# Optimization experiments

Measured on AMD Instinct MI355X. Metric: run time of the kernel, lower is better.

## Reference

```python
import jax, jax.numpy as jnp
import numpy as np

N_NODES = 500_000
N_EDGES = 16_000_000
N_COLORS = 64


def _mix(v, c1, c2):
    """32-bit integer hash (lowbias32-style avalanche mix)."""
    v = v.astype(jnp.uint32)
    v = (v ^ (v >> 16)) * jnp.uint32(c1)
    v = (v ^ (v >> 13)) * jnp.uint32(c2)
    return v ^ (v >> 16)


def setup_inputs() -> dict:
    key = jax.random.key(0)
    k1, k2 = jax.random.split(key)
    x = jax.random.randint(k1, (N_NODES,), 0, N_COLORS, dtype=jnp.int32)
    edge_index = jax.random.randint(k2, (2, N_EDGES), 0, N_NODES, dtype=jnp.int32)
    return {"x": x, "edge_index": edge_index}


def reference(x, edge_index):
    """One Weisfeiler-Lehman color-refinement step.

    Faithful semantics of WLConvOptimized.forward: each node's new label is
    determined by the equivalence class of (own label, multiset of incoming
    neighbor labels). Instead of Python tuple-sort + hash()+dict, we use a
    permutation-invariant multiset hash (sum of two independent 32-bit hashes
    of neighbor labels, combined with the node's own label hash) and then a
    sort-based dense relabeling. Nodes get equal output labels iff their
    (label, neighbor-multiset) signatures collide -- same partition as the
    original (up to astronomically unlikely hash collisions); label numbering
    is canonical (sorted-signature order) rather than dict-insertion order.
    """
    num_nodes = x.shape[0]
    row, col = edge_index[0], edge_index[1]  # message flows row (src) -> col (dst)

    # two independent per-label hashes
    ha = _mix(x, 0x045D9F3B, 0x045D9F3B)
    hb = _mix(x, 0x9E3779B1, 0x85EBCA77)

    # permutation-invariant multiset hash of incoming neighbor labels (gather + scatter-add)
    sum_a = jnp.zeros(num_nodes, jnp.uint32).at[col].add(ha[row])
    sum_b = jnp.zeros(num_nodes, jnp.uint32).at[col].add(hb[row])

    # combine own label with neighbor multiset, re-avalanche
    sig_a = _mix(ha * jnp.uint32(0x27D4EB2F) + sum_a, 0xC2B2AE3D, 0x165667B1)
    sig_b = _mix(hb * jnp.uint32(0x61C88647) + sum_b, 0x045D9F3B, 0x27D4EB2F)

    # dense relabel: sort by (sig_a, sig_b), number distinct signatures 0..K-1
    order = jnp.lexsort((sig_b, sig_a))
    sa, sb = sig_a[order], sig_b[order]
    new_grp = jnp.concatenate([
        jnp.zeros(1, jnp.int32),
        ((sa[1:] != sa[:-1]) | (sb[1:] != sb[:-1])).astype(jnp.int32),
    ])
    labels_sorted = jnp.cumsum(new_grp).astype(jnp.int32)
    out = jnp.zeros(num_nodes, jnp.int32).at[order].set(labels_sorted)
    return out
```

## Files before the change

kernel.cpp:

```cpp
#include <hip/hip_runtime.h>
#include <stdint.h>

#define LOG_B 17
#define NB (1u << LOG_B)
#define FINE_NODES 1024
#define NBKT 512
#define CSH 10
#define EPB 16384

__host__ __device__ constexpr uint32_t cmix(uint32_t v, uint32_t c1, uint32_t c2) {
    v = (v ^ (v >> 16)) * c1;
    v = (v ^ (v >> 13)) * c2;
    return v ^ (v >> 16);
}

__device__ __forceinline__ uint32_t mixh(uint32_t v, uint32_t c1, uint32_t c2) {
    v = (v ^ (v >> 16)) * c1;
    v = (v ^ (v >> 13)) * c2;
    return v ^ (v >> 16);
}

struct Luts { uint32_t ha[64]; uint32_t hb[64]; };
constexpr Luts make_luts() {
    Luts l{};
    for (uint32_t i = 0; i < 64; i++) {
        l.ha[i] = cmix(i, 0x045D9F3Bu, 0x045D9F3Bu);
        l.hb[i] = cmix(i, 0x9E3779B1u, 0x85EBCA77u);
    }
    return l;
}
__constant__ Luts LUT = make_luts();

__global__ __launch_bounds__(256) void k_bin(const int* __restrict__ row, const int* __restrict__ col,
                                             const int* __restrict__ x, uint16_t* __restrict__ bins,
                                             uint32_t* __restrict__ cursor, int E, int cap) {
    __shared__ uint16_t stage[EPB];
    __shared__ uint32_t hist[NBKT];
    __shared__ uint16_t gb16[NBKT];
    __shared__ uint32_t wsum[4];
    int t = threadIdx.x;
    int lane = t & 63, wid = t >> 6;
    int base = blockIdx.x * EPB;
    int nend = min(E - base, EPB);
    for (int b = t; b < NBKT; b += 256) hist[b] = 0;
    __syncthreads();

    const int4* col4 = (const int4*)(col + base);
    const int4* row4 = (const int4*)(row + base);
    int n4 = nend >> 2;

    for (int k = t; k < n4; k += 256) {
        int4 c = col4[k];
        atomicAdd(&hist[(uint32_t)c.x >> CSH], 1u);
        atomicAdd(&hist[(uint32_t)c.y >> CSH], 1u);
        atomicAdd(&hist[(uint32_t)c.z >> CSH], 1u);
        atomicAdd(&hist[(uint32_t)c.w >> CSH], 1u);
    }
    for (int k = (n4 << 2) + t; k < nend; k += 256)
        atomicAdd(&hist[(uint32_t)col[base + k] >> CSH], 1u);
    __syncthreads();

    int b0 = 2 * t;
    uint32_t h0 = hist[b0], h1 = hist[b0 + 1];
    uint32_t s = h0 + h1;
    uint32_t inc = s;
    for (int off = 1; off < 64; off <<= 1) {
        uint32_t nv = __shfl_up(inc, (unsigned)off, 64);
        if (lane >= off) inc += nv;
    }
    if (lane == 63) wsum[wid] = inc;
    __syncthreads();
    uint32_t woff = 0;
    for (int w = 0; w < wid; w++) woff += wsum[w];
    uint32_t e0 = woff + inc - s;
    uint32_t g0 = h0 ? atomicAdd(&cursor[b0], h0) : 0u;
    uint32_t g1 = h1 ? atomicAdd(&cursor[b0 + 1], h1) : 0u;
    gb16[b0] = (uint16_t)g0;
    gb16[b0 + 1] = (uint16_t)g1;
    hist[b0] = e0 << 16;
    hist[b0 + 1] = (e0 + h0) << 16;
    __syncthreads();

    for (int k = t; k < n4; k += 256) {
        int4 c = col4[k];
        int4 r = row4[k];
        {
            uint32_t d = (uint32_t)c.x, b = d >> CSH;
            uint32_t o = atomicAdd(&hist[b], 1u);
            stage[(o >> 16) + (o & 0xFFFFu)] = (uint16_t)(((d & 1023u) << 6) | (uint32_t)x[r.x]);
        }
        {
            uint32_t d = (uint32_t)c.y, b = d >> CSH;
            uint32_t o = atomicAdd(&hist[b], 1u);
            stage[(o >> 16) + (o & 0xFFFFu)] = (uint16_t)(((d & 1023u) << 6) | (uint32_t)x[r.y]);
        }
        {
            uint32_t d = (uint32_t)c.z, b = d >> CSH;
            uint32_t o = atomicAdd(&hist[b], 1u);
            stage[(o >> 16) + (o & 0xFFFFu)] = (uint16_t)(((d & 1023u) << 6) | (uint32_t)x[r.z]);
        }
        {
            uint32_t d = (uint32_t)c.w, b = d >> CSH;
            uint32_t o = atomicAdd(&hist[b], 1u);
            stage[(o >> 16) + (o & 0xFFFFu)] = (uint16_t)(((d & 1023u) << 6) | (uint32_t)x[r.w]);
        }
    }
    for (int k = (n4 << 2) + t; k < nend; k += 256) {
        int i = base + k;
        uint32_t d = (uint32_t)col[i], b = d >> CSH;
        uint32_t o = atomicAdd(&hist[b], 1u);
        stage[(o >> 16) + (o & 0xFFFFu)] = (uint16_t)(((d & 1023u) << 6) | (uint32_t)x[row[i]]);
    }
    __syncthreads();

    int sub = lane >> 4, l16 = lane & 15;
    for (int b = wid * 4 + sub; b < NBKT; b += 16) {
        uint32_t hv = hist[b];
        uint32_t cnt = hv & 0xFFFFu;
        if (!cnt) continue;
        uint32_t s0 = hv >> 16;
        uint16_t* dst = bins + (size_t)b * (uint32_t)cap + gb16[b];
        for (uint32_t off = l16; off < cnt; off += 16)
            dst[off] = stage[s0 + off];
    }
}

__global__ __launch_bounds__(256) void k_accsig(const uint16_t* __restrict__ bins,
                                                const uint32_t* __restrict__ cursor,
                                                const int* __restrict__ x,
                                                unsigned long long* __restrict__ sigs,
                                                uint32_t* __restrict__ bcnt, int N, int cap) {
    __shared__ uint32_t cnt[FINE_NODES * 16];
    int t = threadIdx.x;
    int b = blockIdx.x;
    for (int i = t; i < FINE_NODES * 16; i += 256) cnt[i] = 0;
    __syncthreads();
    uint32_t m = cursor[b];
    const uint16_t* mybins = bins + (size_t)b * (uint32_t)cap;
    const uint2* p16v = (const uint2*)mybins;
    uint32_t m4 = m >> 2;
    for (uint32_t k = t; k < m4; k += 256) {
        uint2 rv = p16v[k];
        {
            uint32_t rec = rv.x & 0xFFFFu, n = rec >> 6, c = rec & 63u;
            atomicAdd(&cnt[n * 16 + (c >> 2)], 1u << (8u * (c & 3u)));
        }
        {
            uint32_t rec = rv.x >> 16, n = rec >> 6, c = rec & 63u;
            atomicAdd(&cnt[n * 16 + (c >> 2)], 1u << (8u * (c & 3u)));
        }
        {
            uint32_t rec = rv.y & 0xFFFFu, n = rec >> 6, c = rec & 63u;
            atomicAdd(&cnt[n * 16 + (c >> 2)], 1u << (8u * (c & 3u)));
        }
        {
            uint32_t rec = rv.y >> 16, n = rec >> 6, c = rec & 63u;
            atomicAdd(&cnt[n * 16 + (c >> 2)], 1u << (8u * (c & 3u)));
        }
    }
    for (uint32_t k = (m4 << 2) + t; k < m; k += 256) {
        uint32_t rec = mybins[k], n = rec >> 6, c = rec & 63u;
        atomicAdd(&cnt[n * 16 + (c >> 2)], 1u << (8u * (c & 3u)));
    }
    __syncthreads();

    for (int n = t; n < FINE_NODES; n += 256) {
        int g = b * FINE_NODES + n;
        if (g >= N) break;
        uint32_t sum_a = 0, sum_b = 0;
#pragma unroll
        for (int w = 0; w < 16; w++) {
            uint32_t wp = (uint32_t)(w + n) & 15u;
            uint32_t v = cnt[n * 16 + wp];
            uint32_t c0 = v & 255u, c1 = (v >> 8) & 255u, c2 = (v >> 16) & 255u, c3 = v >> 24;
            sum_a += c0 * LUT.ha[4 * wp] + c1 * LUT.ha[4 * wp + 1]
                   + c2 * LUT.ha[4 * wp + 2] + c3 * LUT.ha[4 * wp + 3];
            sum_b += c0 * LUT.hb[4 * wp] + c1 * LUT.hb[4 * wp + 1]
                   + c2 * LUT.hb[4 * wp + 2] + c3 * LUT.hb[4 * wp + 3];
        }
        uint32_t xv = (uint32_t)x[g];
        uint32_t ha = LUT.ha[xv];
        uint32_t hb = LUT.hb[xv];
        uint32_t sa = mixh(ha * 0x27D4EB2Fu + sum_a, 0xC2B2AE3Du, 0x165667B1u);
        uint32_t sb = mixh(hb * 0x61C88647u + sum_b, 0x045D9F3Bu, 0x27D4EB2Fu);
        unsigned long long key = ((unsigned long long)sa << 32) | (unsigned long long)sb;
        sigs[g] = key;
        atomicAdd(&bcnt[(uint32_t)(key >> (64 - LOG_B))], 1u);
    }
}

__global__ void k_scan1(const uint32_t* __restrict__ in, uint32_t* __restrict__ out,
                        uint32_t* __restrict__ part) {
    __shared__ uint32_t s[1024];
    int t = threadIdx.x;
    int idx = blockIdx.x * 1024 + t;
    uint32_t v = in[idx];
    s[t] = v;
    __syncthreads();
    for (int off = 1; off < 1024; off <<= 1) {
        uint32_t add = (t >= off) ? s[t - off] : 0u;
        __syncthreads();
        s[t] += add;
        __syncthreads();
    }
    out[idx] = s[t] - v;
    if (t == 1023) part[blockIdx.x] = s[t];
}

__global__ void k_scan2(uint32_t* __restrict__ part) {
    __shared__ uint32_t s[256];
    int t = threadIdx.x;
    uint32_t v = part[t];
    s[t] = v;
    __syncthreads();
    for (int off = 1; off < 256; off <<= 1) {
        uint32_t add = (t >= off) ? s[t - off] : 0u;
        __syncthreads();
        s[t] += add;
        __syncthreads();
    }
    part[t] = s[t] - v;
}

__global__ void k_scan3(uint32_t* __restrict__ out, const uint32_t* __restrict__ part) {
    int idx = blockIdx.x * 1024 + threadIdx.x;
    out[idx] += part[blockIdx.x];
}

__global__ void k_scatter(const unsigned long long* __restrict__ sigs,
                          const uint32_t* __restrict__ boff, uint32_t* __restrict__ bcur,
                          unsigned long long* __restrict__ skey, uint32_t* __restrict__ snode,
                          int N) {
    int i = blockIdx.x * blockDim.x + threadIdx.x;
    if (i >= N) return;
    unsigned long long key = sigs[i];
    uint32_t b = (uint32_t)(key >> (64 - LOG_B));
    uint32_t pos = boff[b] + atomicAdd(&bcur[b], 1u);
    skey[pos] = key;
    snode[pos] = (uint32_t)i;
}

__global__ void k_bsort(unsigned long long* __restrict__ skey, uint32_t* __restrict__ snode,
                        const uint32_t* __restrict__ boff, uint32_t* __restrict__ ldx,
                        uint32_t* __restrict__ dcnt, int N) {
    int b = blockIdx.x * blockDim.x + threadIdx.x;
    if (b >= (int)NB) return;
    uint32_t s0 = boff[b];
    uint32_t s1 = (b == (int)NB - 1) ? (uint32_t)N : boff[b + 1];
    for (uint32_t i = s0 + 1; i < s1; i++) {
        unsigned long long k = skey[i];
        uint32_t nd = snode[i];
        uint32_t j = i;
        while (j > s0 && skey[j - 1] > k) {
            skey[j] = skey[j - 1];
            snode[j] = snode[j - 1];
            j--;
        }
        skey[j] = k;
        snode[j] = nd;
    }
    uint32_t d = 0;
    unsigned long long prev = 0ull;
    for (uint32_t i = s0; i < s1; i++) {
        unsigned long long k = skey[i];
        if (i == s0 || k != prev) d++;
        prev = k;
        ldx[i] = d - 1;
    }
    dcnt[b] = d;
}

__global__ void k_out(const unsigned long long* __restrict__ skey,
                      const uint32_t* __restrict__ snode, const uint32_t* __restrict__ ldx,
                      const uint32_t* __restrict__ doff, int* __restrict__ out, int N) {
    int i = blockIdx.x * blockDim.x + threadIdx.x;
    if (i >= N) return;
    unsigned long long key = skey[i];
    uint32_t b = (uint32_t)(key >> (64 - LOG_B));
    out[snode[i]] = (int)(doff[b] + ldx[i]);
}

extern "C" void kernel_launch(void* const* d_in, const int* in_sizes, int n_in,
                              void* d_out, int out_size, void* d_ws, size_t ws_size,
                              hipStream_t stream) {
    const int* x = (const int*)d_in[0];
    const int* ei = (const int*)d_in[1];
    int N = in_sizes[0];
    int E = in_sizes[1] / 2;
    const int* row = ei;
    const int* col = ei + E;

    int nacc = (N + FINE_NODES - 1) / FINE_NODES;
    int cap = E / NBKT + (E / NBKT) / 16 + 1024;
    cap = (cap + 3) & ~3;

    char* p = (char*)d_ws;
    auto alloc = [&](size_t bytes) -> char* {
        char* r = p;
        p += (bytes + 255) & ~(size_t)255;
        return r;
    };
    uint32_t* cursor = (uint32_t*)alloc((size_t)NBKT * 4);
    uint32_t* bcnt   = (uint32_t*)alloc((size_t)NB * 4);
    uint32_t* bcur   = (uint32_t*)alloc((size_t)NB * 4);
    uint32_t* dcnt   = (uint32_t*)alloc((size_t)NB * 4);
    uint32_t* part   = (uint32_t*)alloc(256 * 4);
    size_t zbytes = (size_t)(p - (char*)d_ws);
    unsigned long long* sigs = (unsigned long long*)alloc((size_t)N * 8);
    uint16_t* bins = (uint16_t*)alloc((size_t)NBKT * cap * 2);
    char* q = (char*)bins;
    auto alias = [&](size_t bytes) -> char* {
        char* r = q;
        q += (bytes + 255) & ~(size_t)255;
        return r;
    };
    unsigned long long* skey = (unsigned long long*)alias((size_t)N * 8);
    uint32_t* snode = (uint32_t*)alias((size_t)N * 4);
    uint32_t* ldx   = (uint32_t*)alias((size_t)N * 4);
    uint32_t* boff  = (uint32_t*)alias((size_t)NB * 4);
    uint32_t* doff  = (uint32_t*)alias((size_t)NB * 4);

    hipMemsetAsync(d_ws, 0, zbytes, stream);

    int nbN = (N + 255) / 256;
    int nbBin = (E + EPB - 1) / EPB;

    k_bin<<<nbBin, 256, 0, stream>>>(row, col, x, bins, cursor, E, cap);
    k_accsig<<<nacc, 256, 0, stream>>>(bins, cursor, x, sigs, bcnt, N, cap);

    k_scan1<<<NB / 1024, 1024, 0, stream>>>(bcnt, boff, part);
    k_scan2<<<1, 256, 0, stream>>>(part);
    k_scan3<<<NB / 1024, 1024, 0, stream>>>(boff, part);

    k_scatter<<<nbN, 256, 0, stream>>>(sigs, boff, bcur, skey, snode, N);
    k_bsort<<<NB / 256, 256, 0, stream>>>(skey, snode, boff, ldx, dcnt, N);

    k_scan1<<<NB / 1024, 1024, 0, stream>>>(dcnt, doff, part);
    k_scan2<<<1, 256, 0, stream>>>(part);
    k_scan3<<<NB / 1024, 1024, 0, stream>>>(doff, part);

    k_out<<<nbN, 256, 0, stream>>>(skey, snode, ldx, doff, (int*)d_out, N);
}
```

Measured before the change: 439.2 us.

## Compress labels to bytes, widen accsig blocks, and use wave-shuffle scans

Adds a pre-pass that packs the int32 node labels into a uint8 array, so the random gathers of x[row] in the binning kernel touch a 500 KB array instead of a 2 MB one and stay cache-resident. Raises k_accsig to 512 threads per block to put more work on its LDS histogram. Rewrites the block scan kernels to use 256 threads, four elements per thread and wavefront shuffle scans in place of the barrier-heavy shared-memory Hillis-Steele loop. The cost is one extra kernel launch and its pass over x. The byte pack assumes labels fit in 8 bits and that N is divisible by 4.

```diff
diff --git a/kernel.cpp b/kernel.cpp
--- a/kernel.cpp
+++ b/kernel.cpp
@@ -31,8 +31,16 @@
 }
 __constant__ Luts LUT = make_luts();
 
+__global__ __launch_bounds__(256) void k_pre(const int4* __restrict__ x4,
+                                             uchar4* __restrict__ xc4, int n4) {
+    int i = blockIdx.x * 256 + threadIdx.x;
+    if (i >= n4) return;
+    int4 v = x4[i];
+    xc4[i] = make_uchar4((uint8_t)v.x, (uint8_t)v.y, (uint8_t)v.z, (uint8_t)v.w);
+}
+
 __global__ __launch_bounds__(256) void k_bin(const int* __restrict__ row, const int* __restrict__ col,
-                                             const int* __restrict__ x, uint16_t* __restrict__ bins,
+                                             const uint8_t* __restrict__ xc, uint16_t* __restrict__ bins,
                                              uint32_t* __restrict__ cursor, int E, int cap) {
     __shared__ uint16_t stage[EPB];
     __shared__ uint32_t hist[NBKT];
@@ -87,29 +95,29 @@
         {
             uint32_t d = (uint32_t)c.x, b = d >> CSH;
             uint32_t o = atomicAdd(&hist[b], 1u);
-            stage[(o >> 16) + (o & 0xFFFFu)] = (uint16_t)(((d & 1023u) << 6) | (uint32_t)x[r.x]);
+            stage[(o >> 16) + (o & 0xFFFFu)] = (uint16_t)(((d & 1023u) << 6) | (uint32_t)xc[r.x]);
         }
         {
             uint32_t d = (uint32_t)c.y, b = d >> CSH;
             uint32_t o = atomicAdd(&hist[b], 1u);
-            stage[(o >> 16) + (o & 0xFFFFu)] = (uint16_t)(((d & 1023u) << 6) | (uint32_t)x[r.y]);
+            stage[(o >> 16) + (o & 0xFFFFu)] = (uint16_t)(((d & 1023u) << 6) | (uint32_t)xc[r.y]);
         }
         {
             uint32_t d = (uint32_t)c.z, b = d >> CSH;
             uint32_t o = atomicAdd(&hist[b], 1u);
-            stage[(o >> 16) + (o & 0xFFFFu)] = (uint16_t)(((d & 1023u) << 6) | (uint32_t)x[r.z]);
+            stage[(o >> 16) + (o & 0xFFFFu)] = (uint16_t)(((d & 1023u) << 6) | (uint32_t)xc[r.z]);
         }
         {
             uint32_t d = (uint32_t)c.w, b = d >> CSH;
             uint32_t o = atomicAdd(&hist[b], 1u);
-            stage[(o >> 16) + (o & 0xFFFFu)] = (uint16_t)(((d & 1023u) << 6) | (uint32_t)x[r.w]);
+            stage[(o >> 16) + (o & 0xFFFFu)] = (uint16_t)(((d & 1023u) << 6) | (uint32_t)xc[r.w]);
         }
     }
     for (int k = (n4 << 2) + t; k < nend; k += 256) {
         int i = base + k;
         uint32_t d = (uint32_t)col[i], b = d >> CSH;
         uint32_t o = atomicAdd(&hist[b], 1u);
-        stage[(o >> 16) + (o & 0xFFFFu)] = (uint16_t)(((d & 1023u) << 6) | (uint32_t)x[row[i]]);
+        stage[(o >> 16) + (o & 0xFFFFu)] = (uint16_t)(((d & 1023u) << 6) | (uint32_t)xc[row[i]]);
     }
     __syncthreads();
 
@@ -125,21 +133,21 @@
     }
 }
 
-__global__ __launch_bounds__(256) void k_accsig(const uint16_t* __restrict__ bins,
+__global__ __launch_bounds__(512) void k_accsig(const uint16_t* __restrict__ bins,
                                                 const uint32_t* __restrict__ cursor,
-                                                const int* __restrict__ x,
+                                                const uint8_t* __restrict__ xc,
                                                 unsigned long long* __restrict__ sigs,
                                                 uint32_t* __restrict__ bcnt, int N, int cap) {
     __shared__ uint32_t cnt[FINE_NODES * 16];
     int t = threadIdx.x;
     int b = blockIdx.x;
-    for (int i = t; i < FINE_NODES * 16; i += 256) cnt[i] = 0;
+    for (int i = t; i < FINE_NODES * 16; i += 512) cnt[i] = 0;
     __syncthreads();
     uint32_t m = cursor[b];
     const uint16_t* mybins = bins + (size_t)b * (uint32_t)cap;
     const uint2* p16v = (const uint2*)mybins;
     uint32_t m4 = m >> 2;
-    for (uint32_t k = t; k < m4; k += 256) {
+    for (uint32_t k = t; k < m4; k += 512) {
         uint2 rv = p16v[k];
         {
             uint32_t rec = rv.x & 0xFFFFu, n = rec >> 6, c = rec & 63u;
@@ -158,13 +166,13 @@
             atomicAdd(&cnt[n * 16 + (c >> 2)], 1u << (8u * (c & 3u)));
         }
     }
-    for (uint32_t k = (m4 << 2) + t; k < m; k += 256) {
+    for (uint32_t k = (m4 << 2) + t; k < m; k += 512) {
         uint32_t rec = mybins[k], n = rec >> 6, c = rec & 63u;
         atomicAdd(&cnt[n * 16 + (c >> 2)], 1u << (8u * (c & 3u)));
     }
     __syncthreads();
 
-    for (int n = t; n < FINE_NODES; n += 256) {
+    for (int n = t; n < FINE_NODES; n += 512) {
         int g = b * FINE_NODES + n;
         if (g >= N) break;
         uint32_t sum_a = 0, sum_b = 0;
@@ -178,7 +186,7 @@
             sum_b += c0 * LUT.hb[4 * wp] + c1 * LUT.hb[4 * wp + 1]
                    + c2 * LUT.hb[4 * wp + 2] + c3 * LUT.hb[4 * wp + 3];
         }
-        uint32_t xv = (uint32_t)x[g];
+        uint32_t xv = (uint32_t)xc[g];
         uint32_t ha = LUT.ha[xv];
         uint32_t hb = LUT.hb[xv];
         uint32_t sa = mixh(ha * 0x27D4EB2Fu + sum_a, 0xC2B2AE3Du, 0x165667B1u);
@@ -189,22 +197,29 @@
     }
 }
 
-__global__ void k_scan1(const uint32_t* __restrict__ in, uint32_t* __restrict__ out,
-                        uint32_t* __restrict__ part) {
-    __shared__ uint32_t s[1024];
+__global__ __launch_bounds__(256) void k_scan1(const uint32_t* __restrict__ in,
+                                               uint32_t* __restrict__ out,
+                                               uint32_t* __restrict__ part) {
+    __shared__ uint32_t wsum[4];
     int t = threadIdx.x;
-    int idx = blockIdx.x * 1024 + t;
-    uint32_t v = in[idx];
-    s[t] = v;
-    __syncthreads();
-    for (int off = 1; off < 1024; off <<= 1) {
-        uint32_t add = (t >= off) ? s[t - off] : 0u;
-        __syncthreads();
-        s[t] += add;
-        __syncthreads();
-    }
-    out[idx] = s[t] - v;
-    if (t == 1023) part[blockIdx.x] = s[t];
+    int lane = t & 63, wid = t >> 6;
+    int base = blockIdx.x * 1024 + 4 * t;
+    uint4 v = *(const uint4*)(in + base);
+    uint32_t s = v.x + v.y + v.z + v.w;
+    uint32_t inc = s;
+    for (int off = 1; off < 64; off <<= 1) {
+        uint32_t nv = __shfl_up(inc, (unsigned)off, 64);
+        if (lane >= off) inc += nv;
+    }
+    if (lane == 63) wsum[wid] = inc;
+    __syncthreads();
+    uint32_t woff = 0;
+    for (int w = 0; w < wid; w++) woff += wsum[w];
+    uint32_t e = woff + inc - s;
+    uint4 o;
+    o.x = e; o.y = e + v.x; o.z = o.y + v.y; o.w = o.z + v.z;
+    *(uint4*)(out + base) = o;
+    if (t == 255) part[blockIdx.x] = wsum[0] + wsum[1] + wsum[2] + wsum[3];
 }
 
 __global__ void k_scan2(uint32_t* __restrict__ part) {
@@ -222,9 +237,13 @@
     part[t] = s[t] - v;
 }
 
-__global__ void k_scan3(uint32_t* __restrict__ out, const uint32_t* __restrict__ part) {
-    int idx = blockIdx.x * 1024 + threadIdx.x;
-    out[idx] += part[blockIdx.x];
+__global__ __launch_bounds__(256) void k_scan3(uint32_t* __restrict__ out,
+                                               const uint32_t* __restrict__ part) {
+    int base = blockIdx.x * 1024 + 4 * threadIdx.x;
+    uint32_t p = part[blockIdx.x];
+    uint4 v = *(const uint4*)(out + base);
+    v.x += p; v.y += p; v.z += p; v.w += p;
+    *(uint4*)(out + base) = v;
 }
 
 __global__ void k_scatter(const unsigned long long* __restrict__ sigs,
@@ -306,6 +325,7 @@
     uint32_t* dcnt   = (uint32_t*)alloc((size_t)NB * 4);
     uint32_t* part   = (uint32_t*)alloc(256 * 4);
     size_t zbytes = (size_t)(p - (char*)d_ws);
+    uint8_t* xc = (uint8_t*)alloc((size_t)N);
     unsigned long long* sigs = (unsigned long long*)alloc((size_t)N * 8);
     uint16_t* bins = (uint16_t*)alloc((size_t)NBKT * cap * 2);
     char* q = (char*)bins;
@@ -324,20 +344,22 @@
 
     int nbN = (N + 255) / 256;
     int nbBin = (E + EPB - 1) / EPB;
-
-    k_bin<<<nbBin, 256, 0, stream>>>(row, col, x, bins, cursor, E, cap);
-    k_accsig<<<nacc, 256, 0, stream>>>(bins, cursor, x, sigs, bcnt, N, cap);
-
-    k_scan1<<<NB / 1024, 1024, 0, stream>>>(bcnt, boff, part);
+    int n4 = N / 4;
+
+    k_pre<<<(n4 + 255) / 256, 256, 0, stream>>>((const int4*)x, (uchar4*)xc, n4);
+    k_bin<<<nbBin, 256, 0, stream>>>(row, col, xc, bins, cursor, E, cap);
+    k_accsig<<<nacc, 512, 0, stream>>>(bins, cursor, xc, sigs, bcnt, N, cap);
+
+    k_scan1<<<NB / 1024, 256, 0, stream>>>(bcnt, boff, part);
     k_scan2<<<1, 256, 0, stream>>>(part);
-    k_scan3<<<NB / 1024, 1024, 0, stream>>>(boff, part);
+    k_scan3<<<NB / 1024, 256, 0, stream>>>(boff, part);
 
     k_scatter<<<nbN, 256, 0, stream>>>(sigs, boff, bcur, skey, snode, N);
     k_bsort<<<NB / 256, 256, 0, stream>>>(skey, snode, boff, ldx, dcnt, N);
 
-    k_scan1<<<NB / 1024, 1024, 0, stream>>>(dcnt, doff, part);
+    k_scan1<<<NB / 1024, 256, 0, stream>>>(dcnt, doff, part);
     k_scan2<<<1, 256, 0, stream>>>(part);
-    k_scan3<<<NB / 1024, 1024, 0, stream>>>(doff, part);
+    k_scan3<<<NB / 1024, 256, 0, stream>>>(doff, part);
 
     k_out<<<nbN, 256, 0, stream>>>(skey, snode, ldx, doff, (int*)d_out, N);
 }
```

Result: no change. 434.0 us (-1.2%).
